# Kernel tuning notes

Hardware: AMD Instinct MI355X
Metric: run time of the kernel (lower is better)

The kernel has to match this reference:

```python
import jax, jax.numpy as jnp
import numpy as np

M, K, N = 8192, 4096, 4096
SCALE_D = 0.05  # per-tensor activation quant step

def setup_inputs() -> dict:
    key = jax.random.key(0)
    k1, k2, k3, k4 = jax.random.split(key, 4)
    x = jax.random.normal(k1, (M, K), jnp.float32)
    # already-quantized int8 weight, stored transposed as in the module: [K, N]
    q_weight = jax.random.randint(k2, (K, N), -127, 128).astype(jnp.int8)
    # per-tensor activation quant: act_scale = 1/scale_d, act_offset = 0
    act_scale = jnp.asarray(1.0 / SCALE_D, jnp.float32)
    act_offset = jnp.asarray(0.0, jnp.float32)
    # per-output-channel weight scales -> deq_scale = scale_d * scale_w, shape [N]
    scale_w = jax.random.uniform(k3, (N,), jnp.float32, 0.001, 0.01)
    deq_scale = (SCALE_D * scale_w).astype(jnp.float32)
    # int32 bias = round(bias_f / (scale_d * scale_w))
    bias_f = jax.random.normal(k4, (N,), jnp.float32) * 0.1
    bias_i32 = jnp.round(bias_f / deq_scale).astype(jnp.int32)
    return {"x": x, "q_weight": q_weight, "act_scale": act_scale,
            "act_offset": act_offset, "deq_scale": deq_scale, "bias_i32": bias_i32}

def reference(x, q_weight, act_scale, act_offset, deq_scale, bias_i32):
    # npu_quantize(div_mode=False): q = clamp(round(x * scale + offset), int8)
    qx = jnp.clip(jnp.round(x * act_scale + act_offset), -128.0, 127.0).astype(jnp.int8)
    # npu_quant_matmul: int8 GEMM accumulated in int32, + int32 bias, * deq_scale
    acc = jnp.matmul(qx.astype(jnp.int32), q_weight.astype(jnp.int32),
                     preferred_element_type=jnp.int32)  # [M, N] int32
    out = (acc + bias_i32[None, :]).astype(jnp.float32) * deq_scale[None, :]
    return out
```

## Files before the change

### kernel.cpp

```cpp
#include <hip/hip_runtime.h>
#include <stdint.h>

#define GM 8192
#define GK 4096
#define GN 4096

typedef int v4i __attribute__((ext_vector_type(4)));

__device__ __forceinline__ void async_load16(const void* gptr, void* lptr) {
  __builtin_amdgcn_global_load_lds(
      (const __attribute__((address_space(1))) void*)gptr,
      (__attribute__((address_space(3))) void*)lptr,
      16 , 0 , 0 );
}

#define TBLK ((GN / 64) * (GK / 64))
#define QBLK (GM * GK / 4 / 256)

__global__ __launch_bounds__(256) void prep_kernel(
    const float* __restrict__ x, int8_t* __restrict__ qx,
    const float* __restrict__ scale_p, const float* __restrict__ off_p,
    const int* __restrict__ B, int8_t* __restrict__ Bt) {
  __shared__ int tile32[64][65];
  const int b = blockIdx.x;
  const int t = threadIdx.x;
  if (b < TBLK) {
    const int n0 = (b & 63) * 64;
    const int k0 = (b >> 6) * 64;
#pragma unroll
    for (int r = 0; r < 4; ++r) {
      const int kl = r * 16 + (t >> 4);
      const int nl = (t & 15) * 4;
      const int4 v = *(const int4*)(B + (size_t)(k0 + kl) * GN + n0 + nl);
      *(int4*)&tile32[kl][nl] = v;
    }
    __syncthreads();
    const int nl = t >> 2;
    const int kc = (t & 3) * 16;
    v4i out;
#pragma unroll
    for (int w = 0; w < 4; ++w) {
      int p = 0;
#pragma unroll
      for (int j = 0; j < 4; ++j)
        p |= (tile32[kc + w * 4 + j][nl] & 0xff) << (8 * j);
      out[w] = p;
    }
    *(v4i*)(Bt + (size_t)(n0 + nl) * GK + k0 + kc) = out;
  } else {
    const int i = (b - TBLK) * 256 + t;
    const float s = scale_p[0], o = off_p[0];
    const float4 f = ((const float4*)x)[i];
    float a0 = fminf(fmaxf(rintf(f.x * s + o), -128.f), 127.f);
    float b0 = fminf(fmaxf(rintf(f.y * s + o), -128.f), 127.f);
    float c0 = fminf(fmaxf(rintf(f.z * s + o), -128.f), 127.f);
    float d0 = fminf(fmaxf(rintf(f.w * s + o), -128.f), 127.f);
    int packed = (((int)a0) & 0xff) | ((((int)b0) & 0xff) << 8) |
                 ((((int)c0) & 0xff) << 16) | ((((int)d0) & 0xff) << 24);
    ((int*)qx)[i] = packed;
  }
}

#define NT (GK / 128)

__global__ __launch_bounds__(512, 2) void gemm_i8_kernel(
    const int8_t* __restrict__ A, const int8_t* __restrict__ Bt,
    const int* __restrict__ bias, const float* __restrict__ deq,
    float* __restrict__ C) {
  __shared__ __align__(16) int8_t Al[2][2][128 * 128];
  __shared__ __align__(16) int8_t Bl[2][2][128 * 128];

  const int t = threadIdx.x;
  const int lane = t & 63;
  const int wid = t >> 6;

  const int bid = blockIdx.x;
  const int swz = (bid & 7) * 64 + (bid >> 3);
  const int m0 = (swz >> 4) * 256;
  const int n0 = (swz & 15) * 256;

  const int ahalf = wid >> 2;
  const int bhalf = (wid & 3) >> 1;
  const int bloc = (wid & 1) * 64;
  const int wm = ahalf * 128;
  const int wn = (wid & 3) * 64;

  const int fr = lane & 15;
  const int kq = lane >> 4;
  const int sw0 = ((kq) ^ (fr & 7)) * 16;
  const int sw1 = ((4 + kq) ^ (fr & 7)) * 16;

  const int srow = t >> 3;
  const int lg16 = (((t & 7) ^ (srow & 7)) * 16);
  const int ldst = t * 16;

  v4i acc[8][4];
  const v4i vz = {0, 0, 0, 0};
#pragma unroll
  for (int m = 0; m < 8; ++m)
#pragma unroll
    for (int n = 0; n < 4; ++n) acc[m][n] = vz;

#define STAGE_TILE(T)                                                  \
  do {                                                                 \
    const int T_ = (T), b_ = T_ & 1;                                   \
    const size_t ko_ = (size_t)T_ * 128 + lg16;                        \
    const int8_t* sa_ = A + (size_t)(m0 + srow) * GK + ko_;            \
    int8_t* da_ = &Al[b_][0][0] + ldst;                                \
    async_load16(sa_, da_);                                            \
    async_load16(sa_ + (size_t)64 * GK, da_ + 8192);                   \
    async_load16(sa_ + (size_t)128 * GK, da_ + 16384);                 \
    async_load16(sa_ + (size_t)192 * GK, da_ + 24576);                 \
    const int8_t* sb_ = Bt + (size_t)(n0 + srow) * GK + ko_;           \
    int8_t* db_ = &Bl[b_][0][0] + ldst;                                \
    async_load16(sb_, db_);                                            \
    async_load16(sb_ + (size_t)64 * GK, db_ + 8192);                   \
    async_load16(sb_ + (size_t)128 * GK, db_ + 16384);                 \
    async_load16(sb_ + (size_t)192 * GK, db_ + 24576);                 \
  } while (0)

#define READ_A(dst, bb, swz_)                                          \
  do {                                                                 \
    const int8_t* p_ = &Al[bb][ahalf][0] + fr * 128 + (swz_);          \
    _Pragma("unroll") for (int i_ = 0; i_ < 8; ++i_)                   \
        dst[i_] = *(const v4i*)(p_ + i_ * 2048);                       \
  } while (0)

#define READ_B(dst, bb, swz_)                                          \
  do {                                                                 \
    const int8_t* p_ = &Bl[bb][bhalf][0] + (bloc + fr) * 128 + (swz_); \
    _Pragma("unroll") for (int i_ = 0; i_ < 4; ++i_)                   \
        dst[i_] = *(const v4i*)(p_ + i_ * 2048);                       \
  } while (0)

#define QUAD(AF, BF, MB)                                               \
  do {                                                                 \
    _Pragma("unroll") for (int mi_ = 0; mi_ < 4; ++mi_) {              \
      _Pragma("unroll") for (int ni_ = 0; ni_ < 4; ++ni_) {            \
        acc[(MB) + mi_][ni_] = __builtin_amdgcn_mfma_i32_16x16x64_i8(  \
            AF[(MB) + mi_], BF[ni_], acc[(MB) + mi_][ni_], 0, 0, 0);   \
      }                                                                \
    }                                                                  \
  } while (0)

  v4i a0[8], b0[4], a1[8], b1[4];

  STAGE_TILE(0);
  asm volatile("s_waitcnt vmcnt(0)\ns_barrier" ::: "memory");
  READ_A(a0, 0, sw0);
  READ_B(b0, 0, sw0);

#pragma unroll 2
  for (int kt = 0; kt < NT - 1; ++kt) {
    const int buf = kt & 1;
    READ_A(a1, buf, sw1);
    READ_B(b1, buf, sw1);
    STAGE_TILE(kt + 1);
    __builtin_amdgcn_s_setprio(1);
    QUAD(a0, b0, 0);
    QUAD(a0, b0, 4);
    __builtin_amdgcn_s_setprio(0);
    asm volatile("s_waitcnt lgkmcnt(0) vmcnt(0)\n\ts_barrier" ::: "memory");
    READ_A(a0, buf ^ 1, sw0);
    READ_B(b0, buf ^ 1, sw0);
    __builtin_amdgcn_s_setprio(1);
    QUAD(a1, b1, 0);
    QUAD(a1, b1, 4);
    __builtin_amdgcn_s_setprio(0);
  }
  {
    const int buf = (NT - 1) & 1;
    READ_A(a1, buf, sw1);
    READ_B(b1, buf, sw1);
    QUAD(a0, b0, 0);
    QUAD(a0, b0, 4);
    QUAD(a1, b1, 0);
    QUAD(a1, b1, 4);
  }

  const int col = lane & 15;
  const int rq = (lane >> 4) * 4;
#pragma unroll
  for (int n = 0; n < 4; ++n) {
    const int gc = n0 + wn + n * 16 + col;
    const float d = deq[gc];
    const int bs = bias[gc];
#pragma unroll
    for (int m = 0; m < 8; ++m) {
      const int gr = m0 + wm + m * 16 + rq;
#pragma unroll
      for (int r = 0; r < 4; ++r)
        C[(size_t)(gr + r) * GN + gc] = (float)(acc[m][n][r] + bs) * d;
    }
  }
#undef STAGE_TILE
#undef READ_A
#undef READ_B
#undef QUAD
}

extern "C" void kernel_launch(void* const* d_in, const int* in_sizes, int n_in,
                              void* d_out, int out_size, void* d_ws, size_t ws_size,
                              hipStream_t stream) {
  const float* x = (const float*)d_in[0];
  const int* qw = (const int*)d_in[1];
  const float* act_scale = (const float*)d_in[2];
  const float* act_offset = (const float*)d_in[3];
  const float* deq = (const float*)d_in[4];
  const int* bias = (const int*)d_in[5];
  float* out = (float*)d_out;

  int8_t* qx = (int8_t*)d_ws;
  int8_t* Bt = (int8_t*)d_ws + (size_t)GM * GK;

  prep_kernel<<<TBLK + QBLK, 256, 0, stream>>>(x, qx, act_scale, act_offset, qw, Bt);
  gemm_i8_kernel<<<dim3((GM / 256) * (GN / 256)), 512, 0, stream>>>(qx, Bt, bias, deq, out);
}
```

Before: 390.6 us.

## Restructure int8 GEMM main loop into four interleaved sub-phases with split prefetch

Breaks each K-tile iteration into four phases that each read a quarter of the LDS fragments, issue a quarter of the next tile's async global-to-LDS loads, and run 16 MFMAs. Barriers and partial vmcnt waits are placed between phases. The goal is to spread memory traffic across the compute and cut register pressure by holding smaller fragment sets. In exchange it adds many more barriers per iteration, which may cost synchronisation time.

```diff
diff --git a/kernel.cpp b/kernel.cpp
--- a/kernel.cpp
+++ b/kernel.cpp
@@ -80,8 +80,6 @@
   const int n0 = (swz & 15) * 256;
 
   const int ahalf = wid >> 2;
-  const int bhalf = (wid & 3) >> 1;
-  const int bloc = (wid & 1) * 64;
   const int wm = ahalf * 128;
   const int wn = (wid & 3) * 64;
 
@@ -101,81 +99,105 @@
 #pragma unroll
     for (int n = 0; n < 4; ++n) acc[m][n] = vz;
 
-#define STAGE_TILE(T)                                                  \
-  do {                                                                 \
-    const int T_ = (T), b_ = T_ & 1;                                   \
-    const size_t ko_ = (size_t)T_ * 128 + lg16;                        \
-    const int8_t* sa_ = A + (size_t)(m0 + srow) * GK + ko_;            \
-    int8_t* da_ = &Al[b_][0][0] + ldst;                                \
-    async_load16(sa_, da_);                                            \
-    async_load16(sa_ + (size_t)64 * GK, da_ + 8192);                   \
-    async_load16(sa_ + (size_t)128 * GK, da_ + 16384);                 \
-    async_load16(sa_ + (size_t)192 * GK, da_ + 24576);                 \
-    const int8_t* sb_ = Bt + (size_t)(n0 + srow) * GK + ko_;           \
-    int8_t* db_ = &Bl[b_][0][0] + ldst;                                \
-    async_load16(sb_, db_);                                            \
-    async_load16(sb_ + (size_t)64 * GK, db_ + 8192);                   \
-    async_load16(sb_ + (size_t)128 * GK, db_ + 16384);                 \
-    async_load16(sb_ + (size_t)192 * GK, db_ + 24576);                 \
-  } while (0)
-
-#define READ_A(dst, bb, swz_)                                          \
-  do {                                                                 \
-    const int8_t* p_ = &Al[bb][ahalf][0] + fr * 128 + (swz_);          \
-    _Pragma("unroll") for (int i_ = 0; i_ < 8; ++i_)                   \
-        dst[i_] = *(const v4i*)(p_ + i_ * 2048);                       \
-  } while (0)
-
-#define READ_B(dst, bb, swz_)                                          \
-  do {                                                                 \
-    const int8_t* p_ = &Bl[bb][bhalf][0] + (bloc + fr) * 128 + (swz_); \
+#define STAGE_AQ(T_, q_)                                               \
+  do {                                                                 \
+    const int8_t* s_ = A + (size_t)(m0 + (q_) * 64 + srow) * GK +      \
+                       (size_t)(T_) * 128 + lg16;                      \
+    async_load16(s_, &Al[(T_) & 1][0][0] + (q_) * 8192 + ldst);        \
+  } while (0)
+#define STAGE_BQ(T_, q_)                                               \
+  do {                                                                 \
+    const int8_t* s_ = Bt + (size_t)(n0 + (q_) * 64 + srow) * GK +     \
+                       (size_t)(T_) * 128 + lg16;                      \
+    async_load16(s_, &Bl[(T_) & 1][0][0] + (q_) * 8192 + ldst);        \
+  } while (0)
+
+#define READ_A4(dst, mh_, swz_)                                        \
+  do {                                                                 \
+    const int8_t* p_ = &Al[buf][0][0] +                                \
+        (size_t)(wm + (mh_) * 64 + fr) * 128 + (swz_);                 \
     _Pragma("unroll") for (int i_ = 0; i_ < 4; ++i_)                   \
         dst[i_] = *(const v4i*)(p_ + i_ * 2048);                       \
   } while (0)
-
-#define QUAD(AF, BF, MB)                                               \
+#define READ_B4(dst, swz_)                                             \
+  do {                                                                 \
+    const int8_t* p_ = &Bl[buf][0][0] + (size_t)(wn + fr) * 128 + (swz_); \
+    _Pragma("unroll") for (int i_ = 0; i_ < 4; ++i_)                   \
+        dst[i_] = *(const v4i*)(p_ + i_ * 2048);                       \
+  } while (0)
+
+#define QUAD16(AF, BF, MB)                                             \
   do {                                                                 \
     _Pragma("unroll") for (int mi_ = 0; mi_ < 4; ++mi_) {              \
       _Pragma("unroll") for (int ni_ = 0; ni_ < 4; ++ni_) {            \
         acc[(MB) + mi_][ni_] = __builtin_amdgcn_mfma_i32_16x16x64_i8(  \
-            AF[(MB) + mi_], BF[ni_], acc[(MB) + mi_][ni_], 0, 0, 0);   \
+            AF[mi_], BF[ni_], acc[(MB) + mi_][ni_], 0, 0, 0);          \
       }                                                                \
     }                                                                  \
   } while (0)
 
-  v4i a0[8], b0[4], a1[8], b1[4];
-
-  STAGE_TILE(0);
-  asm volatile("s_waitcnt vmcnt(0)\ns_barrier" ::: "memory");
-  READ_A(a0, 0, sw0);
-  READ_B(b0, 0, sw0);
+#define LGKM0 asm volatile("s_waitcnt lgkmcnt(0)" ::: "memory")
+#define VMC4 asm volatile("s_waitcnt vmcnt(4)" ::: "memory")
+#define VMC2 asm volatile("s_waitcnt vmcnt(2)" ::: "memory")
+#define VMC0 asm volatile("s_waitcnt vmcnt(0)" ::: "memory")
+#define BAR __builtin_amdgcn_s_barrier()
+#define PRIO1 __builtin_amdgcn_s_setprio(1)
+#define PRIO0 __builtin_amdgcn_s_setprio(0)
+
+  v4i aL0[4], aL1[4], aH0[4], aH1[4], bK0[4], bK1[4];
+
+  STAGE_AQ(0, 0); STAGE_AQ(0, 2);
+  STAGE_BQ(0, 0); STAGE_BQ(0, 1); STAGE_BQ(0, 2); STAGE_BQ(0, 3);
+  STAGE_AQ(0, 1); STAGE_AQ(0, 3);
+  VMC0;
+  BAR;
 
 #pragma unroll 2
   for (int kt = 0; kt < NT - 1; ++kt) {
     const int buf = kt & 1;
-    READ_A(a1, buf, sw1);
-    READ_B(b1, buf, sw1);
-    STAGE_TILE(kt + 1);
-    __builtin_amdgcn_s_setprio(1);
-    QUAD(a0, b0, 0);
-    QUAD(a0, b0, 4);
-    __builtin_amdgcn_s_setprio(0);
-    asm volatile("s_waitcnt lgkmcnt(0) vmcnt(0)\n\ts_barrier" ::: "memory");
-    READ_A(a0, buf ^ 1, sw0);
-    READ_B(b0, buf ^ 1, sw0);
-    __builtin_amdgcn_s_setprio(1);
-    QUAD(a1, b1, 0);
-    QUAD(a1, b1, 4);
-    __builtin_amdgcn_s_setprio(0);
+    READ_A4(aL0, 0, sw0);
+    READ_B4(bK0, sw0);
+    STAGE_AQ(kt + 1, 0); STAGE_AQ(kt + 1, 2);
+    BAR;
+    LGKM0;
+    PRIO1; QUAD16(aL0, bK0, 0); PRIO0;
+    BAR;
+    READ_A4(aL1, 0, sw1);
+    READ_B4(bK1, sw1);
+    STAGE_BQ(kt + 1, 0); STAGE_BQ(kt + 1, 1);
+    BAR;
+    LGKM0;
+    PRIO1; QUAD16(aL1, bK1, 0); PRIO0;
+    VMC4;
+    BAR;
+    READ_A4(aH0, 1, sw0);
+    STAGE_BQ(kt + 1, 2); STAGE_BQ(kt + 1, 3);
+    BAR;
+    LGKM0;
+    PRIO1; QUAD16(aH0, bK0, 4); PRIO0;
+    BAR;
+    READ_A4(aH1, 1, sw1);
+    STAGE_AQ(kt + 1, 1); STAGE_AQ(kt + 1, 3);
+    BAR;
+    LGKM0;
+    PRIO1; QUAD16(aH1, bK1, 4); PRIO0;
+    VMC2;
+    BAR;
   }
   {
     const int buf = (NT - 1) & 1;
-    READ_A(a1, buf, sw1);
-    READ_B(b1, buf, sw1);
-    QUAD(a0, b0, 0);
-    QUAD(a0, b0, 4);
-    QUAD(a1, b1, 0);
-    QUAD(a1, b1, 4);
+    READ_A4(aL0, 0, sw0);
+    READ_B4(bK0, sw0);
+    READ_A4(aL1, 0, sw1);
+    READ_B4(bK1, sw1);
+    QUAD16(aL0, bK0, 0);
+    QUAD16(aL1, bK1, 0);
+    VMC0;
+    BAR;
+    READ_A4(aH0, 1, sw0);
+    READ_A4(aH1, 1, sw1);
+    QUAD16(aH0, bK0, 4);
+    QUAD16(aH1, bK1, 4);
   }
 
   const int col = lane & 15;
@@ -193,10 +215,18 @@
         C[(size_t)(gr + r) * GN + gc] = (float)(acc[m][n][r] + bs) * d;
     }
   }
-#undef STAGE_TILE
-#undef READ_A
-#undef READ_B
-#undef QUAD
+#undef STAGE_AQ
+#undef STAGE_BQ
+#undef READ_A4
+#undef READ_B4
+#undef QUAD16
+#undef LGKM0
+#undef VMC4
+#undef VMC2
+#undef VMC0
+#undef BAR
+#undef PRIO1
+#undef PRIO0
 }
 
 extern "C" void kernel_launch(void* const* d_in, const int* in_sizes, int n_in,
```

New measurement: 391.6 us. About the same (+0.2%).
